# Kernel tuning notes

Hardware: AMD Instinct MI355X
Metric: run time of the kernel (lower is better)

The kernel has to match this reference:

```python
import jax, jax.numpy as jnp
import numpy as np

N_TETS, C, D = 1_000_000, 32, 8
N_FACES = 400_000


def setup_inputs() -> dict:
    key = jax.random.key(0)
    features = jax.random.normal(key, (N_TETS, C, D), dtype=jnp.float32)
    # disjoint face pairs: arange gives all-distinct tet indices (< N_TETS)
    faces = jnp.arange(N_FACES * 2, dtype=jnp.int64).reshape(N_FACES, 2)
    return {"features": features, "faces": faces}


def reference(features, faces):
    # Per-tet max over the local feature axis D: [n_tets, C]
    base = jnp.max(features, axis=-1)
    # For each sampled face, max over concat([tet1, tet2], dim=-1) ==
    # elementwise max of the two per-tet maxima. Gather both endpoints.
    f1 = base[faces[:, 0]]            # [n_faces, C]
    f2 = base[faces[:, 1]]            # [n_faces, C]
    shared = jnp.maximum(f1, f2)      # [n_faces, C]
    # Scatter shared features back to both tets (faces are disjoint, no races)
    out = base.at[faces[:, 0]].set(shared).at[faces[:, 1]].set(shared)
    return out
```

## Files before the change

### kernel.cpp

```cpp
#include <hip/hip_runtime.h>


__global__ void partner_init_kernel(int* __restrict__ partner, int n) {
    int stride = gridDim.x * blockDim.x;
    for (int i = blockIdx.x * blockDim.x + threadIdx.x; i < n; i += stride)
        partner[i] = -1;
}

__global__ void partner_build_kernel(const int* __restrict__ faces,
                                     int* __restrict__ partner, int n_faces) {
    int stride = gridDim.x * blockDim.x;
    for (int f = blockIdx.x * blockDim.x + threadIdx.x; f < n_faces; f += stride) {
        int a = faces[2 * f];
        int b = faces[2 * f + 1];
        partner[a] = b;
        partner[b] = a;
    }
}

__device__ __forceinline__ float max8(float4 a, float4 b) {
    return fmaxf(fmaxf(fmaxf(a.x, a.y), fmaxf(a.z, a.w)),
                 fmaxf(fmaxf(b.x, b.y), fmaxf(b.z, b.w)));
}

__global__ void fused_pool_kernel(const float* __restrict__ feat,
                                  const int* __restrict__ partner,
                                  float* __restrict__ out, int n4) {
    int stride = gridDim.x * blockDim.x;
    for (int t = blockIdx.x * blockDim.x + threadIdx.x; t < n4; t += stride) {
        int row = t >> 3;
        int c4  = (t & 7) << 2;
        const float4* p =
            reinterpret_cast<const float4*>(feat + (size_t)row * 256 + (size_t)c4 * 8);
        float m[4];
#pragma unroll
        for (int j = 0; j < 4; ++j)
            m[j] = max8(p[2 * j], p[2 * j + 1]);

        int pr = partner[row];

        float pm[4];
#pragma unroll
        for (int j = 0; j < 4; ++j)
            pm[j] = __shfl_xor(m[j], 8, 64);

        if (pr >= 0) {
            if (pr == (row ^ 1)) {
#pragma unroll
                for (int j = 0; j < 4; ++j)
                    m[j] = fmaxf(m[j], pm[j]);
            } else {
                const float4* q = reinterpret_cast<const float4*>(
                    feat + (size_t)pr * 256 + (size_t)c4 * 8);
#pragma unroll
                for (int j = 0; j < 4; ++j)
                    m[j] = fmaxf(m[j], max8(q[2 * j], q[2 * j + 1]));
            }
        }

        float4 o = make_float4(m[0], m[1], m[2], m[3]);
        *reinterpret_cast<float4*>(out + (size_t)t * 4) = o;
    }
}


__global__ void base_max_kernel(const float* __restrict__ feat,
                                float* __restrict__ out, int n) {
    int stride = gridDim.x * blockDim.x;
    for (int i = blockIdx.x * blockDim.x + threadIdx.x; i < n; i += stride) {
        const float4* p = reinterpret_cast<const float4*>(feat + (size_t)i * 8);
        out[i] = max8(p[0], p[1]);
    }
}

__global__ void face_share_kernel(const int* __restrict__ faces,
                                  float* __restrict__ out, int n_faces) {
    int total = n_faces * 8;
    int stride = gridDim.x * blockDim.x;
    for (int t = blockIdx.x * blockDim.x + threadIdx.x; t < total; t += stride) {
        int face = t >> 3;
        int c4   = (t & 7) << 2;
        size_t f1 = (size_t)faces[2 * face];
        size_t f2 = (size_t)faces[2 * face + 1];
        float* p1 = out + f1 * 32 + c4;
        float* p2 = out + f2 * 32 + c4;
        float4 v1 = *reinterpret_cast<const float4*>(p1);
        float4 v2 = *reinterpret_cast<const float4*>(p2);
        float4 s;
        s.x = fmaxf(v1.x, v2.x);
        s.y = fmaxf(v1.y, v2.y);
        s.z = fmaxf(v1.z, v2.z);
        s.w = fmaxf(v1.w, v2.w);
        *reinterpret_cast<float4*>(p1) = s;
        *reinterpret_cast<float4*>(p2) = s;
    }
}

extern "C" void kernel_launch(void* const* d_in, const int* in_sizes, int n_in,
                              void* d_out, int out_size, void* d_ws, size_t ws_size,
                              hipStream_t stream) {
    const float* feat  = (const float*)d_in[0];
    const int*   faces = (const int*)d_in[1];
    float* out = (float*)d_out;

    const int n_elems = out_size;
    const int n_rows  = out_size / 32;
    const int n_faces = in_sizes[1] / 2;

    const int block = 256;
    const size_t partner_bytes = (size_t)n_rows * sizeof(int);

    if (ws_size >= partner_bytes) {
        int* partner = (int*)d_ws;

        int grid_i = min((n_rows + block - 1) / block, 2048);
        partner_init_kernel<<<grid_i, block, 0, stream>>>(partner, n_rows);

        int grid_f = min((n_faces + block - 1) / block, 2048);
        partner_build_kernel<<<grid_f, block, 0, stream>>>(faces, partner, n_faces);

        int n4 = n_elems / 4;
        int grid_m = min((n4 + block - 1) / block, 4096);
        fused_pool_kernel<<<grid_m, block, 0, stream>>>(feat, partner, out, n4);
    } else {
        int grid_a = min((n_elems + block - 1) / block, 4096);
        base_max_kernel<<<grid_a, block, 0, stream>>>(feat, out, n_elems);

        int grid_b = min((n_faces * 8 + block - 1) / block, 4096);
        face_share_kernel<<<grid_b, block, 0, stream>>>(faces, out, n_faces);
    }
}
```

Measured before the change: 251.6 us.

## Remap fused pool kernel so each wave reads contiguous 2KB chunks coalesced

```diff
diff --git a/kernel.cpp b/kernel.cpp
--- a/kernel.cpp
+++ b/kernel.cpp
@@ -18,48 +18,50 @@
     }
 }
 
+__device__ __forceinline__ float max4(float4 a) {
+    return fmaxf(fmaxf(a.x, a.y), fmaxf(a.z, a.w));
+}
 __device__ __forceinline__ float max8(float4 a, float4 b) {
-    return fmaxf(fmaxf(fmaxf(a.x, a.y), fmaxf(a.z, a.w)),
-                 fmaxf(fmaxf(b.x, b.y), fmaxf(b.z, b.w)));
+    return fmaxf(max4(a), max4(b));
 }
 
 __global__ void fused_pool_kernel(const float* __restrict__ feat,
                                   const int* __restrict__ partner,
-                                  float* __restrict__ out, int n4) {
-    int stride = gridDim.x * blockDim.x;
-    for (int t = blockIdx.x * blockDim.x + threadIdx.x; t < n4; t += stride) {
-        int row = t >> 3;
-        int c4  = (t & 7) << 2;
-        const float4* p =
-            reinterpret_cast<const float4*>(feat + (size_t)row * 256 + (size_t)c4 * 8);
-        float m[4];
-#pragma unroll
-        for (int j = 0; j < 4; ++j)
-            m[j] = max8(p[2 * j], p[2 * j + 1]);
+                                  float* __restrict__ out, int n_chunks) {
+    int lane     = threadIdx.x & 63;
+    int wave     = (blockIdx.x * blockDim.x + threadIdx.x) >> 6;
+    int n_waves  = (gridDim.x * blockDim.x) >> 6;
 
-        int pr = partner[row];
+    for (int chunk = wave; chunk < n_chunks; chunk += n_waves) {
+        const float* base = feat + (size_t)chunk * 512;
+        float4 v0 = *reinterpret_cast<const float4*>(base + lane * 4);
+        float4 v1 = *reinterpret_cast<const float4*>(base + 256 + lane * 4);
 
-        float pm[4];
-#pragma unroll
-        for (int j = 0; j < 4; ++j)
-            pm[j] = __shfl_xor(m[j], 8, 64);
+        float m0 = max4(v0);
+        float m1 = max4(v1);
+        float p0 = fmaxf(m0, __shfl_xor(m0, 1, 64));
+        float p1 = fmaxf(m1, __shfl_xor(m1, 1, 64));
+        int l2 = (2 * lane) & 63;
+        float a = __shfl(p0, l2, 64);
+        float b = __shfl(p1, l2, 64);
+        float r = (lane < 32) ? a : b;
 
+        int rc  = chunk * 64 + lane;
+        int row = rc >> 5;
+        int pr  = partner[row];
+
+        float rp = __shfl_xor(r, 32, 64);
         if (pr >= 0) {
             if (pr == (row ^ 1)) {
-#pragma unroll
-                for (int j = 0; j < 4; ++j)
-                    m[j] = fmaxf(m[j], pm[j]);
+                r = fmaxf(r, rp);
             } else {
+                int c = rc & 31;
                 const float4* q = reinterpret_cast<const float4*>(
-                    feat + (size_t)pr * 256 + (size_t)c4 * 8);
-#pragma unroll
-                for (int j = 0; j < 4; ++j)
-                    m[j] = fmaxf(m[j], max8(q[2 * j], q[2 * j + 1]));
+                    feat + ((size_t)pr * 32 + c) * 8);
+                r = fmaxf(r, max8(q[0], q[1]));
             }
         }
-
-        float4 o = make_float4(m[0], m[1], m[2], m[3]);
-        *reinterpret_cast<float4*>(out + (size_t)t * 4) = o;
+        out[rc] = r;
     }
 }
 
@@ -110,7 +112,7 @@
     const int block = 256;
     const size_t partner_bytes = (size_t)n_rows * sizeof(int);
 
-    if (ws_size >= partner_bytes) {
+    if (ws_size >= partner_bytes && (n_elems & 63) == 0) {
         int* partner = (int*)d_ws;
 
         int grid_i = min((n_rows + block - 1) / block, 2048);
@@ -119,9 +121,9 @@
         int grid_f = min((n_faces + block - 1) / block, 2048);
         partner_build_kernel<<<grid_f, block, 0, stream>>>(faces, partner, n_faces);
 
-        int n4 = n_elems / 4;
-        int grid_m = min((n4 + block - 1) / block, 4096);
-        fused_pool_kernel<<<grid_m, block, 0, stream>>>(feat, partner, out, n4);
+        int n_chunks = n_elems / 64;
+        int grid_m = min((n_chunks + 3) / 4, 4096);
+        fused_pool_kernel<<<grid_m, block, 0, stream>>>(feat, partner, out, n_chunks);
     } else {
         int grid_a = min((n_elems + block - 1) / block, 4096);
         base_max_kernel<<<grid_a, block, 0, stream>>>(feat, out, n_elems);
```

New measurement: 253.4 us. Within noise of the previous version (+0.7%).
